# Optimization experiments

Measured on AMD Instinct MI355X. Metric: run time of the kernel, lower is better.

The kernel has to match this reference:

```python
import jax, jax.numpy as jnp
import numpy as np

N = 100000   # nodes
E = 1600000  # edges (avg degree 16)
F_IN = 128   # num_features
H = 128      # num_hidden
C = 40       # num_classes


def setup_inputs() -> dict:
    key = jax.random.key(0)
    ks = jax.random.split(key, 8)
    w = lambda k, sh: jax.random.normal(k, sh, dtype=jnp.float32) * 0.05
    return {
        "x": jax.random.normal(ks[0], (N, F_IN), dtype=jnp.float32),
        "edge_index": jax.random.randint(ks[1], (2, E), 0, N),
        "W_rel1": w(ks[2], (F_IN, H)),
        "b_rel1": jnp.zeros((H,), jnp.float32),
        "W_root1": w(ks[3], (F_IN, H)),
        "W_rel2": w(ks[4], (H, H)),
        "b_rel2": jnp.zeros((H,), jnp.float32),
        "W_root2": w(ks[5], (H, H)),
        "W_lin": w(ks[6], (2 * H, C)),
        "b_lin": jnp.zeros((C,), jnp.float32),
    }


def _graph_conv(x, src, dst, W_rel, b_rel, W_root, n):
    # PyG GraphConv: sum_{j in N(i)} x_j -> lin_rel, plus lin_root(x_i)
    agg = jax.ops.segment_sum(x[src], dst, num_segments=n)  # [N, d_in]
    return agg @ W_rel + b_rel + x @ W_root


def reference(x, edge_index, W_rel1, b_rel1, W_root1, W_rel2, b_rel2, W_root2, W_lin, b_lin):
    src, dst = edge_index[0], edge_index[1]
    n = x.shape[0]
    # dropout is identity at inference (training=False)
    x1 = jax.nn.relu(_graph_conv(x, src, dst, W_rel1, b_rel1, W_root1, n))
    x2 = jax.nn.relu(_graph_conv(x1, src, dst, W_rel2, b_rel2, W_root2, n))
    h = jnp.concatenate([x1, x2], axis=-1)  # [N, 2H]
    return jax.nn.log_softmax(h @ W_lin + b_lin, axis=-1)
```

## Files before the change

kernel.cpp:

```cpp
#include <hip/hip_runtime.h>
#include <hip/hip_bf16.h>

typedef __attribute__((ext_vector_type(8))) short bf16x8;
typedef __attribute__((ext_vector_type(4))) float f32x4;

#define EPB 4096
#define BUCKET_BITS 8
#define BUCKET_SIZE 256
#define MAXBUCK 512

static __device__ __forceinline__ unsigned short f2bf(float f) {
    union { float f; unsigned u; } v; v.f = f;
    unsigned r = v.u + 0x7FFF + ((v.u >> 16) & 1);
    return (unsigned short)(r >> 16);
}
static __device__ __forceinline__ float asf(unsigned u) {
    union { unsigned u; float f; } v; v.u = u;
    return v.f;
}

__global__ __launch_bounds__(256) void prep(const float* __restrict__ Wrel1,
                                            const float* __restrict__ Wroot1,
                                            const float* __restrict__ Wrel2,
                                            const float* __restrict__ Wroot2,
                                            const float* __restrict__ Wlin,
                                            const int* __restrict__ dst,
                                            unsigned short* __restrict__ bsw1,
                                            unsigned short* __restrict__ bsw2,
                                            unsigned short* __restrict__ bswL,
                                            int* __restrict__ hist,
                                            int E, int nblk, int nbuck) {
    __shared__ int h[MAXBUCK];
    int blk = blockIdx.x, t = threadIdx.x;
    if (blk < 256) {
        const float* Wrel  = (blk < 128) ? Wrel1 : Wrel2;
        const float* Wroot = (blk < 128) ? Wroot1 : Wroot2;
        unsigned short* bsw = (blk < 128) ? bsw1 : bsw2;
        int idx = (blk & 127) * 256 + t;
        int j = idx & 7, L = (idx >> 3) & 63, ct = (idx >> 9) & 15, kt = idx >> 13;
        int k = kt * 32 + ((L >> 4) * 8) + j;
        int c = ct * 16 + (L & 15);
        float v = (c < 128) ? Wrel[k * 128 + c] : Wroot[k * 128 + (c - 128)];
        bsw[idx] = f2bf(v);
    } else if (blk < 304) {
        int idx = (blk - 256) * 256 + t;
        int tt = idx;
        int j = tt & 7; tt >>= 3;
        int L = tt & 63; tt >>= 6;
        int ct = tt % 3;
        int kt = tt / 3;
        int k = kt * 32 + ((L >> 4) * 8) + j;
        int c = ct * 16 + (L & 15);
        float v = (c < 40) ? Wlin[k * 40 + c] : 0.f;
        bswL[idx] = f2bf(v);
    } else {
        int hb = blk - 304;
        for (int i = t; i < MAXBUCK; i += 256) h[i] = 0;
        __syncthreads();
        int e0 = hb * EPB;
#pragma unroll
        for (int it = 0; it < EPB / 256; it++) {
            int e = e0 + it * 256 + t;
            if (e < E) atomicAdd(&h[dst[e] >> BUCKET_BITS], 1);
        }
        __syncthreads();
        for (int i = t; i < nbuck; i += 256) hist[i * nblk + hb] = h[i];
    }
}

__global__ __launch_bounds__(256) void bucket_total(const int* __restrict__ hist,
                                                    int* __restrict__ total, int nblk) {
    __shared__ int s[256];
    int b = blockIdx.x, t = threadIdx.x;
    int v = 0;
    for (int i = t; i < nblk; i += 256) v += hist[b * nblk + i];
    s[t] = v; __syncthreads();
#pragma unroll
    for (int o = 128; o >= 1; o >>= 1) {
        if (t < o) s[t] += s[t + o];
        __syncthreads();
    }
    if (t == 0) total[b] = s[0];
}

__global__ __launch_bounds__(256) void bucket_scan(const int* __restrict__ total,
                                                   int* __restrict__ base, int nbuck) {
    __shared__ int s[256];
    int t = threadIdx.x;
    int e0 = (2 * t < nbuck) ? total[2 * t] : 0;
    int e1 = (2 * t + 1 < nbuck) ? total[2 * t + 1] : 0;
    int ps = e0 + e1;
    s[t] = ps; __syncthreads();
#pragma unroll
    for (int o = 1; o < 256; o <<= 1) {
        int x = (t >= o) ? s[t - o] : 0;
        __syncthreads();
        s[t] += x; __syncthreads();
    }
    int pbase = s[t] - ps;
    if (2 * t <= nbuck) base[2 * t] = pbase;
    if (2 * t + 1 <= nbuck) base[2 * t + 1] = pbase + e0;
}

__global__ __launch_bounds__(256) void block_scan(int* __restrict__ hist,
                                                  const int* __restrict__ base, int nblk) {
    __shared__ int s[256];
    int b = blockIdx.x, t = threadIdx.x;
    int carryv = base[b];
    for (int start = 0; start < nblk; start += 256) {
        int i = start + t;
        int v = (i < nblk) ? hist[b * nblk + i] : 0;
        s[t] = v; __syncthreads();
#pragma unroll
        for (int o = 1; o < 256; o <<= 1) {
            int x = (t >= o) ? s[t - o] : 0;
            __syncthreads();
            s[t] += x; __syncthreads();
        }
        int excl = s[t] - v + carryv;
        if (i < nblk) hist[b * nblk + i] = excl;
        carryv += s[255];
        __syncthreads();
    }
}

__global__ __launch_bounds__(256) void edge_part(const int* __restrict__ src,
                                                 const int* __restrict__ dst,
                                                 const int* __restrict__ hist,
                                                 int* __restrict__ part,
                                                 int E, int nblk, int nbuck) {
    __shared__ int hcnt[MAXBUCK];
    __shared__ int lstart[MAXBUCK];
    __shared__ int cur[MAXBUCK];
    __shared__ int gbase[MAXBUCK];
    __shared__ int s2[256];
    __shared__ int sdst[EPB];
    __shared__ int ssrc[EPB];
    int t = threadIdx.x, blk = blockIdx.x;
    int e0 = blk * EPB;
    int cnt = E - e0; if (cnt > EPB) cnt = EPB;
    for (int i = t; i < MAXBUCK; i += 256) hcnt[i] = 0;
    for (int i = t; i < nbuck; i += 256) gbase[i] = hist[i * nblk + blk];
    __syncthreads();
    int myd[EPB / 256], mys[EPB / 256];
#pragma unroll
    for (int it = 0; it < EPB / 256; it++) {
        int i = it * 256 + t;
        if (i < cnt) {
            myd[it] = dst[e0 + i];
            mys[it] = src[e0 + i];
            atomicAdd(&hcnt[myd[it] >> BUCKET_BITS], 1);
        }
    }
    __syncthreads();
    int p0 = hcnt[2 * t], p1 = hcnt[2 * t + 1];
    int ps = p0 + p1;
    s2[t] = ps; __syncthreads();
#pragma unroll
    for (int o = 1; o < 256; o <<= 1) {
        int x = (t >= o) ? s2[t - o] : 0;
        __syncthreads();
        s2[t] += x; __syncthreads();
    }
    int pbase = s2[t] - ps;
    lstart[2 * t] = pbase; lstart[2 * t + 1] = pbase + p0;
    cur[2 * t] = 0; cur[2 * t + 1] = 0;
    __syncthreads();
#pragma unroll
    for (int it = 0; it < EPB / 256; it++) {
        int i = it * 256 + t;
        if (i < cnt) {
            int b = myd[it] >> BUCKET_BITS;
            int p = lstart[b] + atomicAdd(&cur[b], 1);
            sdst[p] = myd[it];
            ssrc[p] = mys[it];
        }
    }
    __syncthreads();
    for (int i = t; i < cnt; i += 256) {
        int d = sdst[i], s = ssrc[i];
        int b = d >> BUCKET_BITS;
        part[gbase[b] + (i - lstart[b])] = ((d & (BUCKET_SIZE - 1)) << 17) | s;
    }
}

__global__ __launch_bounds__(256) void csrfin_gemm1(const int* __restrict__ part,
                                                    const int* __restrict__ bucketBase,
                                                    int* __restrict__ off_,
                                                    int* __restrict__ deg_,
                                                    int* __restrict__ csr_src,
                                                    const float* __restrict__ x,
                                                    const unsigned short* __restrict__ Bsw,
                                                    const float* __restrict__ bias,
                                                    unsigned short* __restrict__ xr,
                                                    unsigned short* __restrict__ accbf,
                                                    int N, int nbuck) {
    __shared__ int cur[BUCKET_SIZE];
    __shared__ int h[BUCKET_SIZE];
    __shared__ int tsum[256];
    int t = threadIdx.x;
    if (blockIdx.x < (unsigned)nbuck) {
        int b = blockIdx.x;
        int lo = bucketBase[b], hi = bucketBase[b + 1];
        int n0 = b * BUCKET_SIZE;
        h[t] = 0;
        __syncthreads();
        for (int i = lo + t; i < hi; i += 256) atomicAdd(&h[part[i] >> 17], 1);
        __syncthreads();
        int hv = h[t];
        tsum[t] = hv;
        __syncthreads();
#pragma unroll
        for (int o = 1; o < 256; o <<= 1) {
            int xx = (t >= o) ? tsum[t - o] : 0;
            __syncthreads();
            tsum[t] += xx;
            __syncthreads();
        }
        int st = tsum[t] - hv;
        cur[t] = st;
        int node = n0 + t;
        if (node < N) { off_[node] = lo + st; deg_[node] = hv; }
        __syncthreads();
        for (int i = lo + t; i < hi; i += 256) {
            int rec = part[i];
            int p = atomicAdd(&cur[rec >> 17], 1);
            csr_src[lo + p] = rec & 0x1FFFF;
        }
    } else {
        int wid = (blockIdx.x - nbuck) * 4 + (t >> 6);
        int L = t & 63;
        int r0 = wid * 16;
        if (r0 >= N) return;
        int arow = r0 + (L & 15);
        const bf16x8* Bptr = ((const bf16x8*)Bsw) + L;
        f32x4 acc[16];
#pragma unroll
        for (int i = 0; i < 16; i++) acc[i] = (f32x4){0.f, 0.f, 0.f, 0.f};
#pragma unroll
        for (int kt = 0; kt < 4; kt++) {
            const float* Arow = x + (size_t)arow * 128 + ((L >> 4) * 8) + kt * 32;
            float4 a0 = *(const float4*)Arow;
            float4 a1 = *(const float4*)(Arow + 4);
            bf16x8 a;
            a[0] = (short)f2bf(a0.x); a[1] = (short)f2bf(a0.y);
            a[2] = (short)f2bf(a0.z); a[3] = (short)f2bf(a0.w);
            a[4] = (short)f2bf(a1.x); a[5] = (short)f2bf(a1.y);
            a[6] = (short)f2bf(a1.z); a[7] = (short)f2bf(a1.w);
#pragma unroll
            for (int ct = 0; ct < 16; ct++) {
                bf16x8 b = Bptr[(kt * 16 + ct) * 64];
                acc[ct] = __builtin_amdgcn_mfma_f32_16x16x32_bf16(a, b, acc[ct], 0, 0, 0);
            }
        }
        int rbase = r0 + (L >> 4) * 4;
        int cl = L & 15;
#pragma unroll
        for (int ct = 0; ct < 16; ct++) {
            int col = ct * 16 + cl;
#pragma unroll
            for (int r = 0; r < 4; r++) {
                int row = rbase + r;
                float v = acc[ct][r];
                if (col < 128)
                    xr[(size_t)row * 128 + col] = f2bf(v);
                else
                    accbf[(size_t)row * 128 + (col - 128)] = f2bf(v + bias[col - 128]);
            }
        }
    }
}

__global__ __launch_bounds__(256) void gemm_layer2(const unsigned short* __restrict__ Abf,
                                                   const unsigned short* __restrict__ Bsw,
                                                   const float* __restrict__ bias,
                                                   unsigned short* __restrict__ xr,
                                                   unsigned short* __restrict__ accbf, int N) {
    int wid = blockIdx.x * 4 + (threadIdx.x >> 6);
    int L = threadIdx.x & 63;
    int r0 = wid * 16;
    if (r0 >= N) return;
    int arow = r0 + (L & 15);
    const bf16x8* Bptr = ((const bf16x8*)Bsw) + L;
    f32x4 acc[16];
#pragma unroll
    for (int i = 0; i < 16; i++) acc[i] = (f32x4){0.f, 0.f, 0.f, 0.f};
#pragma unroll
    for (int kt = 0; kt < 4; kt++) {
        bf16x8 a = *((const bf16x8*)(Abf + (size_t)arow * 128 + ((L >> 4) * 8) + kt * 32));
#pragma unroll
        for (int ct = 0; ct < 16; ct++) {
            bf16x8 b = Bptr[(kt * 16 + ct) * 64];
            acc[ct] = __builtin_amdgcn_mfma_f32_16x16x32_bf16(a, b, acc[ct], 0, 0, 0);
        }
    }
    int rbase = r0 + (L >> 4) * 4;
    int cl = L & 15;
#pragma unroll
    for (int ct = 0; ct < 16; ct++) {
        int col = ct * 16 + cl;
#pragma unroll
        for (int r = 0; r < 4; r++) {
            int row = rbase + r;
            float v = acc[ct][r];
            if (col < 128)
                xr[(size_t)row * 128 + col] = f2bf(v);
            else
                accbf[(size_t)row * 128 + (col - 128)] = f2bf(v + bias[col - 128]);
        }
    }
}

__global__ __launch_bounds__(256) void agg_relu_cvt(const unsigned short* __restrict__ xr,
                                                    const unsigned short* __restrict__ accbf,
                                                    const int* __restrict__ off_,
                                                    const int* __restrict__ deg,
                                                    const int* __restrict__ csr_src,
                                                    unsigned short* __restrict__ out, int N) {
    int node = blockIdx.x * 4 + (threadIdx.x >> 6);
    if (node >= N) return;
    int L = threadIdx.x & 63;
    int g = L >> 4;
    int f = L & 15;
    int o = off_[node];
    int d = deg[node];
    uint4 arow = (uint4){0, 0, 0, 0};
    if (g == 0) arow = *(const uint4*)(accbf + (size_t)node * 128 + f * 8);

    const int* ip = csr_src + o + g;
    const unsigned short* xrf = xr + f * 8;

    float lo0 = 0.f, lo1 = 0.f, lo2 = 0.f, lo3 = 0.f;
    float hi0 = 0.f, hi1 = 0.f, hi2 = 0.f, hi3 = 0.f;

    int d4 = d & ~3;
#pragma unroll 4
    for (int k = 0; k < d4; k += 4) {
        int s = ip[k];
        uint4 p = *(const uint4*)(xrf + (size_t)s * 128);
        lo0 += asf(p.x << 16); hi0 += asf(p.x & 0xFFFF0000u);
        lo1 += asf(p.y << 16); hi1 += asf(p.y & 0xFFFF0000u);
        lo2 += asf(p.z << 16); hi2 += asf(p.z & 0xFFFF0000u);
        lo3 += asf(p.w << 16); hi3 += asf(p.w & 0xFFFF0000u);
    }
    if (d4 + g < d) {
        int s = ip[d4];
        uint4 p = *(const uint4*)(xrf + (size_t)s * 128);
        lo0 += asf(p.x << 16); hi0 += asf(p.x & 0xFFFF0000u);
        lo1 += asf(p.y << 16); hi1 += asf(p.y & 0xFFFF0000u);
        lo2 += asf(p.z << 16); hi2 += asf(p.z & 0xFFFF0000u);
        lo3 += asf(p.w << 16); hi3 += asf(p.w & 0xFFFF0000u);
    }
    lo0 += __shfl_xor(lo0, 16, 64); hi0 += __shfl_xor(hi0, 16, 64);
    lo1 += __shfl_xor(lo1, 16, 64); hi1 += __shfl_xor(hi1, 16, 64);
    lo2 += __shfl_xor(lo2, 16, 64); hi2 += __shfl_xor(hi2, 16, 64);
    lo3 += __shfl_xor(lo3, 16, 64); hi3 += __shfl_xor(hi3, 16, 64);
    lo0 += __shfl_xor(lo0, 32, 64); hi0 += __shfl_xor(hi0, 32, 64);
    lo1 += __shfl_xor(lo1, 32, 64); hi1 += __shfl_xor(hi1, 32, 64);
    lo2 += __shfl_xor(lo2, 32, 64); hi2 += __shfl_xor(hi2, 32, 64);
    lo3 += __shfl_xor(lo3, 32, 64); hi3 += __shfl_xor(hi3, 32, 64);

    if (g == 0) {
        uint4 wv;
        wv.x = ((unsigned)f2bf(fmaxf(asf(arow.x & 0xFFFF0000u) + hi0, 0.f)) << 16)
             | f2bf(fmaxf(asf(arow.x << 16) + lo0, 0.f));
        wv.y = ((unsigned)f2bf(fmaxf(asf(arow.y & 0xFFFF0000u) + hi1, 0.f)) << 16)
             | f2bf(fmaxf(asf(arow.y << 16) + lo1, 0.f));
        wv.z = ((unsigned)f2bf(fmaxf(asf(arow.z & 0xFFFF0000u) + hi2, 0.f)) << 16)
             | f2bf(fmaxf(asf(arow.z << 16) + lo2, 0.f));
        wv.w = ((unsigned)f2bf(fmaxf(asf(arow.w & 0xFFFF0000u) + hi3, 0.f)) << 16)
             | f2bf(fmaxf(asf(arow.w << 16) + lo3, 0.f));
        *(uint4*)(out + (size_t)node * 128 + f * 8) = wv;
    }
}

__global__ __launch_bounds__(256) void gemm_final_ls(const unsigned short* __restrict__ x1bf,
                                                     const unsigned short* __restrict__ x2bf,
                                                     const unsigned short* __restrict__ Bsw,
                                                     const float* __restrict__ blin,
                                                     float* __restrict__ out, int N) {
    int wid = blockIdx.x * 4 + (threadIdx.x >> 6);
    int L = threadIdx.x & 63;
    int r0 = wid * 16;
    if (r0 >= N) return;
    int arow = r0 + (L & 15);
    f32x4 acc[3];
#pragma unroll
    for (int i = 0; i < 3; i++) acc[i] = (f32x4){0.f, 0.f, 0.f, 0.f};
#pragma unroll
    for (int kt = 0; kt < 8; kt++) {
        const unsigned short* Ab = (kt < 4) ? x1bf : x2bf;
        int kk = (kt & 3) * 32 + ((L >> 4) * 8);
        bf16x8 a = *((const bf16x8*)(Ab + (size_t)arow * 128 + kk));
#pragma unroll
        for (int ct = 0; ct < 3; ct++) {
            bf16x8 b = ((const bf16x8*)Bsw)[(kt * 3 + ct) * 64 + L];
            acc[ct] = __builtin_amdgcn_mfma_f32_16x16x32_bf16(a, b, acc[ct], 0, 0, 0);
        }
    }
    int rbase = r0 + (L >> 4) * 4;
    int cl = L & 15;
    float b0 = blin[cl], b1 = blin[16 + cl];
    float b2 = (cl < 8) ? blin[32 + cl] : 0.f;
#pragma unroll
    for (int r = 0; r < 4; r++) {
        int row = rbase + r;
        float v0 = acc[0][r] + b0;
        float v1 = acc[1][r] + b1;
        float v2 = (cl < 8) ? (acc[2][r] + b2) : -__builtin_inff();
        float m = fmaxf(fmaxf(v0, v1), v2);
#pragma unroll
        for (int off = 8; off >= 1; off >>= 1) m = fmaxf(m, __shfl_xor(m, off, 64));
        float e = __expf(v0 - m) + __expf(v1 - m) + ((cl < 8) ? __expf(v2 - m) : 0.f);
#pragma unroll
        for (int off = 8; off >= 1; off >>= 1) e += __shfl_xor(e, off, 64);
        float ls = m + __logf(e);
        float* op = out + (size_t)row * 40;
        op[cl] = v0 - ls;
        op[16 + cl] = v1 - ls;
        if (cl < 8) op[32 + cl] = v2 - ls;
    }
}

extern "C" void kernel_launch(void* const* d_in, const int* in_sizes, int n_in,
                              void* d_out, int out_size, void* d_ws, size_t ws_size,
                              hipStream_t stream) {
    const float* x      = (const float*)d_in[0];
    const int*   edge   = (const int*)d_in[1];
    const float* Wrel1  = (const float*)d_in[2];
    const float* brel1  = (const float*)d_in[3];
    const float* Wroot1 = (const float*)d_in[4];
    const float* Wrel2  = (const float*)d_in[5];
    const float* brel2  = (const float*)d_in[6];
    const float* Wroot2 = (const float*)d_in[7];
    const float* Wlin   = (const float*)d_in[8];
    const float* blin   = (const float*)d_in[9];

    const int N = in_sizes[0] / 128;
    const int E = in_sizes[1] / 2;
    const int* src = edge;
    const int* dst = edge + E;

    const int nblk  = (E + EPB - 1) / EPB;
    const int nbuck = (N + BUCKET_SIZE - 1) / BUCKET_SIZE;

    char* ws = (char*)d_ws;
    size_t off = 0;
    auto alloc = [&](size_t bytes) -> void* {
        void* p = ws + off;
        off += (bytes + 255) & ~(size_t)255;
        return p;
    };
    unsigned short* x1bf = (unsigned short*)alloc((size_t)N * 128 * 2);
    unsigned short* x2bf = (unsigned short*)alloc((size_t)N * 128 * 2);
    unsigned short* xr   = (unsigned short*)alloc((size_t)N * 128 * 2);
    unsigned short* accbf= (unsigned short*)alloc((size_t)N * 128 * 2);
    unsigned short* bsw1 = (unsigned short*)alloc(32768 * 2);
    unsigned short* bsw2 = (unsigned short*)alloc(32768 * 2);
    unsigned short* bswL = (unsigned short*)alloc(12288 * 2);
    int* hist       = (int*)alloc((size_t)nbuck * nblk * 4);
    int* bucketTot  = (int*)alloc((size_t)nbuck * 4);
    int* bucketBase = (int*)alloc((size_t)(nbuck + 1) * 4);
    int* part       = (int*)alloc((size_t)E * 4);
    int* csr_src    = (int*)alloc((size_t)E * 4);
    int* off_       = (int*)alloc((size_t)N * 4);
    int* deg_       = (int*)alloc((size_t)N * 4);

    const int rowTiles = (N + 15) / 16;
    const int gemmBlocks = (rowTiles + 3) / 4;
    const int nodeBlocks = (N + 3) / 4;

    prep<<<304 + nblk, 256, 0, stream>>>(Wrel1, Wroot1, Wrel2, Wroot2, Wlin, dst,
                                         bsw1, bsw2, bswL, hist, E, nblk, nbuck);
    bucket_total<<<nbuck, 256, 0, stream>>>(hist, bucketTot, nblk);
    bucket_scan<<<1, 256, 0, stream>>>(bucketTot, bucketBase, nbuck);
    block_scan<<<nbuck, 256, 0, stream>>>(hist, bucketBase, nblk);
    edge_part<<<nblk, 256, 0, stream>>>(src, dst, hist, part, E, nblk, nbuck);
    csrfin_gemm1<<<nbuck + gemmBlocks, 256, 0, stream>>>(part, bucketBase, off_, deg_, csr_src,
                                                         x, bsw1, brel1, xr, accbf, N, nbuck);
    agg_relu_cvt<<<nodeBlocks, 256, 0, stream>>>(xr, accbf, off_, deg_, csr_src, x1bf, N);
    gemm_layer2<<<gemmBlocks, 256, 0, stream>>>(x1bf, bsw2, brel2, xr, accbf, N);
    agg_relu_cvt<<<nodeBlocks, 256, 0, stream>>>(xr, accbf, off_, deg_, csr_src, x2bf, N);
    gemm_final_ls<<<gemmBlocks, 256, 0, stream>>>(x1bf, x2bf, bswL, blin, (float*)d_out, N);
}
```

Baseline: 346.1 us.

## Stage GEMM weights in LDS with persistent grid-stride tiles; vectorize bf16 accumulation

gemm_layer2 and gemm_final_ls now copy the pre-swizzled weight matrix into shared memory once per block. They then loop over row tiles with a fixed grid of 512 persistent blocks, instead of launching one block per four tiles that each re-read the weights from global memory. The aggregation kernel packs its lo/hi bf16 accumulators into float2 vectors, which may let the compiler emit packed adds. In exchange, the layer-2 GEMM takes 64KB of LDS per block, which limits occupancy, and the fixed grid size may underfill or unbalance the GPU.

Measured after the change: 336.4 us. -2.8%, faster.

```diff
diff --git a/kernel.cpp b/kernel.cpp
--- a/kernel.cpp
+++ b/kernel.cpp
@@ -3,6 +3,7 @@
 
 typedef __attribute__((ext_vector_type(8))) short bf16x8;
 typedef __attribute__((ext_vector_type(4))) float f32x4;
+typedef __attribute__((ext_vector_type(2))) float f32x2;
 
 #define EPB 4096
 #define BUCKET_BITS 8
@@ -17,6 +18,12 @@
 static __device__ __forceinline__ float asf(unsigned u) {
     union { unsigned u; float f; } v; v.u = u;
     return v.f;
+}
+static __device__ __forceinline__ f32x2 cvt2(unsigned u) {
+    f32x2 r;
+    r.x = asf(u << 16);
+    r.y = asf(u & 0xFFFF0000u);
+    return r;
 }
 
 __global__ __launch_bounds__(256) void prep(const float* __restrict__ Wrel1,
@@ -276,37 +283,46 @@
                                                    const float* __restrict__ bias,
                                                    unsigned short* __restrict__ xr,
                                                    unsigned short* __restrict__ accbf, int N) {
-    int wid = blockIdx.x * 4 + (threadIdx.x >> 6);
-    int L = threadIdx.x & 63;
-    int r0 = wid * 16;
-    if (r0 >= N) return;
-    int arow = r0 + (L & 15);
-    const bf16x8* Bptr = ((const bf16x8*)Bsw) + L;
-    f32x4 acc[16];
-#pragma unroll
-    for (int i = 0; i < 16; i++) acc[i] = (f32x4){0.f, 0.f, 0.f, 0.f};
-#pragma unroll
-    for (int kt = 0; kt < 4; kt++) {
-        bf16x8 a = *((const bf16x8*)(Abf + (size_t)arow * 128 + ((L >> 4) * 8) + kt * 32));
+    __shared__ unsigned short Bs[32768];
+    int t = threadIdx.x;
+    {
+        uint4* d4 = (uint4*)Bs;
+        const uint4* s4 = (const uint4*)Bsw;
+#pragma unroll
+        for (int i = 0; i < 16; i++) d4[t + i * 256] = s4[t + i * 256];
+    }
+    __syncthreads();
+    int w = t >> 6, L = t & 63;
+    int nTiles = (N + 15) / 16;
+    for (int tile = blockIdx.x * 4 + w; tile < nTiles; tile += gridDim.x * 4) {
+        int r0 = tile * 16;
+        int arow = r0 + (L & 15);
+        f32x4 acc[16];
+#pragma unroll
+        for (int i = 0; i < 16; i++) acc[i] = (f32x4){0.f, 0.f, 0.f, 0.f};
+#pragma unroll
+        for (int kt = 0; kt < 4; kt++) {
+            bf16x8 a = *((const bf16x8*)(Abf + (size_t)arow * 128 + ((L >> 4) * 8) + kt * 32));
+#pragma unroll
+            for (int ct = 0; ct < 16; ct++) {
+                bf16x8 b = *(const bf16x8*)(Bs + (((kt * 16 + ct) * 64) + L) * 8);
+                acc[ct] = __builtin_amdgcn_mfma_f32_16x16x32_bf16(a, b, acc[ct], 0, 0, 0);
+            }
+        }
+        int rbase = r0 + (L >> 4) * 4;
+        int cl = L & 15;
 #pragma unroll
         for (int ct = 0; ct < 16; ct++) {
-            bf16x8 b = Bptr[(kt * 16 + ct) * 64];
-            acc[ct] = __builtin_amdgcn_mfma_f32_16x16x32_bf16(a, b, acc[ct], 0, 0, 0);
-        }
-    }
-    int rbase = r0 + (L >> 4) * 4;
-    int cl = L & 15;
-#pragma unroll
-    for (int ct = 0; ct < 16; ct++) {
-        int col = ct * 16 + cl;
-#pragma unroll
-        for (int r = 0; r < 4; r++) {
-            int row = rbase + r;
-            float v = acc[ct][r];
-            if (col < 128)
-                xr[(size_t)row * 128 + col] = f2bf(v);
-            else
-                accbf[(size_t)row * 128 + (col - 128)] = f2bf(v + bias[col - 128]);
+            int col = ct * 16 + cl;
+#pragma unroll
+            for (int r = 0; r < 4; r++) {
+                int row = rbase + r;
+                float v = acc[ct][r];
+                if (col < 128)
+                    xr[(size_t)row * 128 + col] = f2bf(v);
+                else
+                    accbf[(size_t)row * 128 + (col - 128)] = f2bf(v + bias[col - 128]);
+            }
         }
     }
 }
@@ -330,46 +346,46 @@
     const int* ip = csr_src + o + g;
     const unsigned short* xrf = xr + f * 8;
 
-    float lo0 = 0.f, lo1 = 0.f, lo2 = 0.f, lo3 = 0.f;
-    float hi0 = 0.f, hi1 = 0.f, hi2 = 0.f, hi3 = 0.f;
+    f32x2 a0 = (f32x2){0.f, 0.f}, a1 = (f32x2){0.f, 0.f};
+    f32x2 a2 = (f32x2){0.f, 0.f}, a3 = (f32x2){0.f, 0.f};
 
     int d4 = d & ~3;
 #pragma unroll 4
     for (int k = 0; k < d4; k += 4) {
         int s = ip[k];
         uint4 p = *(const uint4*)(xrf + (size_t)s * 128);
-        lo0 += asf(p.x << 16); hi0 += asf(p.x & 0xFFFF0000u);
-        lo1 += asf(p.y << 16); hi1 += asf(p.y & 0xFFFF0000u);
-        lo2 += asf(p.z << 16); hi2 += asf(p.z & 0xFFFF0000u);
-        lo3 += asf(p.w << 16); hi3 += asf(p.w & 0xFFFF0000u);
+        a0 += cvt2(p.x);
+        a1 += cvt2(p.y);
+        a2 += cvt2(p.z);
+        a3 += cvt2(p.w);
     }
     if (d4 + g < d) {
         int s = ip[d4];
         uint4 p = *(const uint4*)(xrf + (size_t)s * 128);
-        lo0 += asf(p.x << 16); hi0 += asf(p.x & 0xFFFF0000u);
-        lo1 += asf(p.y << 16); hi1 += asf(p.y & 0xFFFF0000u);
-        lo2 += asf(p.z << 16); hi2 += asf(p.z & 0xFFFF0000u);
-        lo3 += asf(p.w << 16); hi3 += asf(p.w & 0xFFFF0000u);
-    }
-    lo0 += __shfl_xor(lo0, 16, 64); hi0 += __shfl_xor(hi0, 16, 64);
-    lo1 += __shfl_xor(lo1, 16, 64); hi1 += __shfl_xor(hi1, 16, 64);
-    lo2 += __shfl_xor(lo2, 16, 64); hi2 += __shfl_xor(hi2, 16, 64);
-    lo3 += __shfl_xor(lo3, 16, 64); hi3 += __shfl_xor(hi3, 16, 64);
-    lo0 += __shfl_xor(lo0, 32, 64); hi0 += __shfl_xor(hi0, 32, 64);
-    lo1 += __shfl_xor(lo1, 32, 64); hi1 += __shfl_xor(hi1, 32, 64);
-    lo2 += __shfl_xor(lo2, 32, 64); hi2 += __shfl_xor(hi2, 32, 64);
-    lo3 += __shfl_xor(lo3, 32, 64); hi3 += __shfl_xor(hi3, 32, 64);
+        a0 += cvt2(p.x);
+        a1 += cvt2(p.y);
+        a2 += cvt2(p.z);
+        a3 += cvt2(p.w);
+    }
+    a0.x += __shfl_xor(a0.x, 16, 64); a0.y += __shfl_xor(a0.y, 16, 64);
+    a1.x += __shfl_xor(a1.x, 16, 64); a1.y += __shfl_xor(a1.y, 16, 64);
+    a2.x += __shfl_xor(a2.x, 16, 64); a2.y += __shfl_xor(a2.y, 16, 64);
+    a3.x += __shfl_xor(a3.x, 16, 64); a3.y += __shfl_xor(a3.y, 16, 64);
+    a0.x += __shfl_xor(a0.x, 32, 64); a0.y += __shfl_xor(a0.y, 32, 64);
+    a1.x += __shfl_xor(a1.x, 32, 64); a1.y += __shfl_xor(a1.y, 32, 64);
+    a2.x += __shfl_xor(a2.x, 32, 64); a2.y += __shfl_xor(a2.y, 32, 64);
+    a3.x += __shfl_xor(a3.x, 32, 64); a3.y += __shfl_xor(a3.y, 32, 64);
 
     if (g == 0) {
         uint4 wv;
-        wv.x = ((unsigned)f2bf(fmaxf(asf(arow.x & 0xFFFF0000u) + hi0, 0.f)) << 16)
-             | f2bf(fmaxf(asf(arow.x << 16) + lo0, 0.f));
-        wv.y = ((unsigned)f2bf(fmaxf(asf(arow.y & 0xFFFF0000u) + hi1, 0.f)) << 16)
-             | f2bf(fmaxf(asf(arow.y << 16) + lo1, 0.f));
-        wv.z = ((unsigned)f2bf(fmaxf(asf(arow.z & 0xFFFF0000u) + hi2, 0.f)) << 16)
-             | f2bf(fmaxf(asf(arow.z << 16) + lo2, 0.f));
-        wv.w = ((unsigned)f2bf(fmaxf(asf(arow.w & 0xFFFF0000u) + hi3, 0.f)) << 16)
-             | f2bf(fmaxf(asf(arow.w << 16) + lo3, 0.f));
+        wv.x = ((unsigned)f2bf(fmaxf(asf(arow.x & 0xFFFF0000u) + a0.y, 0.f)) << 16)
+             | f2bf(fmaxf(asf(arow.x << 16) + a0.x, 0.f));
+        wv.y = ((unsigned)f2bf(fmaxf(asf(arow.y & 0xFFFF0000u) + a1.y, 0.f)) << 16)
+             | f2bf(fmaxf(asf(arow.y << 16) + a1.x, 0.f));
+        wv.z = ((unsigned)f2bf(fmaxf(asf(arow.z & 0xFFFF0000u) + a2.y, 0.f)) << 16)
+             | f2bf(fmaxf(asf(arow.z << 16) + a2.x, 0.f));
+        wv.w = ((unsigned)f2bf(fmaxf(asf(arow.w & 0xFFFF0000u) + a3.y, 0.f)) << 16)
+             | f2bf(fmaxf(asf(arow.w << 16) + a3.x, 0.f));
         *(uint4*)(out + (size_t)node * 128 + f * 8) = wv;
     }
 }
@@ -379,46 +395,56 @@
                                                      const unsigned short* __restrict__ Bsw,
                                                      const float* __restrict__ blin,
                                                      float* __restrict__ out, int N) {
-    int wid = blockIdx.x * 4 + (threadIdx.x >> 6);
-    int L = threadIdx.x & 63;
-    int r0 = wid * 16;
-    if (r0 >= N) return;
-    int arow = r0 + (L & 15);
-    f32x4 acc[3];
-#pragma unroll
-    for (int i = 0; i < 3; i++) acc[i] = (f32x4){0.f, 0.f, 0.f, 0.f};
-#pragma unroll
-    for (int kt = 0; kt < 8; kt++) {
-        const unsigned short* Ab = (kt < 4) ? x1bf : x2bf;
-        int kk = (kt & 3) * 32 + ((L >> 4) * 8);
-        bf16x8 a = *((const bf16x8*)(Ab + (size_t)arow * 128 + kk));
-#pragma unroll
-        for (int ct = 0; ct < 3; ct++) {
-            bf16x8 b = ((const bf16x8*)Bsw)[(kt * 3 + ct) * 64 + L];
-            acc[ct] = __builtin_amdgcn_mfma_f32_16x16x32_bf16(a, b, acc[ct], 0, 0, 0);
-        }
-    }
-    int rbase = r0 + (L >> 4) * 4;
+    __shared__ unsigned short Bs[12288];
+    int t = threadIdx.x;
+    {
+        uint4* d4 = (uint4*)Bs;
+        const uint4* s4 = (const uint4*)Bsw;
+#pragma unroll
+        for (int i = 0; i < 6; i++) d4[t + i * 256] = s4[t + i * 256];
+    }
+    __syncthreads();
+    int w = t >> 6, L = t & 63;
     int cl = L & 15;
     float b0 = blin[cl], b1 = blin[16 + cl];
     float b2 = (cl < 8) ? blin[32 + cl] : 0.f;
-#pragma unroll
-    for (int r = 0; r < 4; r++) {
-        int row = rbase + r;
-        float v0 = acc[0][r] + b0;
-        float v1 = acc[1][r] + b1;
-        float v2 = (cl < 8) ? (acc[2][r] + b2) : -__builtin_inff();
-        float m = fmaxf(fmaxf(v0, v1), v2);
-#pragma unroll
-        for (int off = 8; off >= 1; off >>= 1) m = fmaxf(m, __shfl_xor(m, off, 64));
-        float e = __expf(v0 - m) + __expf(v1 - m) + ((cl < 8) ? __expf(v2 - m) : 0.f);
-#pragma unroll
-        for (int off = 8; off >= 1; off >>= 1) e += __shfl_xor(e, off, 64);
-        float ls = m + __logf(e);
-        float* op = out + (size_t)row * 40;
-        op[cl] = v0 - ls;
-        op[16 + cl] = v1 - ls;
-        if (cl < 8) op[32 + cl] = v2 - ls;
+    int nTiles = (N + 15) / 16;
+    for (int tile = blockIdx.x * 4 + w; tile < nTiles; tile += gridDim.x * 4) {
+        int r0 = tile * 16;
+        int arow = r0 + (L & 15);
+        f32x4 acc[3];
+#pragma unroll
+        for (int i = 0; i < 3; i++) acc[i] = (f32x4){0.f, 0.f, 0.f, 0.f};
+#pragma unroll
+        for (int kt = 0; kt < 8; kt++) {
+            const unsigned short* Ab = (kt < 4) ? x1bf : x2bf;
+            int kk = (kt & 3) * 32 + ((L >> 4) * 8);
+            bf16x8 a = *((const bf16x8*)(Ab + (size_t)arow * 128 + kk));
+#pragma unroll
+            for (int ct = 0; ct < 3; ct++) {
+                bf16x8 b = *(const bf16x8*)(Bs + (((kt * 3 + ct) * 64) + L) * 8);
+                acc[ct] = __builtin_amdgcn_mfma_f32_16x16x32_bf16(a, b, acc[ct], 0, 0, 0);
+            }
+        }
+        int rbase = r0 + (L >> 4) * 4;
+#pragma unroll
+        for (int r = 0; r < 4; r++) {
+            int row = rbase + r;
+            float v0 = acc[0][r] + b0;
+            float v1 = acc[1][r] + b1;
+            float v2 = (cl < 8) ? (acc[2][r] + b2) : -__builtin_inff();
+            float m = fmaxf(fmaxf(v0, v1), v2);
+#pragma unroll
+            for (int off = 8; off >= 1; off >>= 1) m = fmaxf(m, __shfl_xor(m, off, 64));
+            float e = __expf(v0 - m) + __expf(v1 - m) + ((cl < 8) ? __expf(v2 - m) : 0.f);
+#pragma unroll
+            for (int off = 8; off >= 1; off >>= 1) e += __shfl_xor(e, off, 64);
+            float ls = m + __logf(e);
+            float* op = out + (size_t)row * 40;
+            op[cl] = v0 - ls;
+            op[16 + cl] = v1 - ls;
+            if (cl < 8) op[32 + cl] = v2 - ls;
+        }
     }
 }
 
@@ -479,7 +505,7 @@
     csrfin_gemm1<<<nbuck + gemmBlocks, 256, 0, stream>>>(part, bucketBase, off_, deg_, csr_src,
                                                          x, bsw1, brel1, xr, accbf, N, nbuck);
     agg_relu_cvt<<<nodeBlocks, 256, 0, stream>>>(xr, accbf, off_, deg_, csr_src, x1bf, N);
-    gemm_layer2<<<gemmBlocks, 256, 0, stream>>>(x1bf, bsw2, brel2, xr, accbf, N);
+    gemm_layer2<<<512, 256, 0, stream>>>(x1bf, bsw2, brel2, xr, accbf, N);
     agg_relu_cvt<<<nodeBlocks, 256, 0, stream>>>(xr, accbf, off_, deg_, csr_src, x2bf, N);
-    gemm_final_ls<<<gemmBlocks, 256, 0, stream>>>(x1bf, x2bf, bswL, blin, (float*)d_out, N);
-}
+    gemm_final_ls<<<512, 256, 0, stream>>>(x1bf, x2bf, bswL, blin, (float*)d_out, N);
+}
```
